# Kernel tuning notes

Measured on AMD Instinct MI355X. Metric: run time of the kernel, lower is better.

Reference implementation:

```python
import jax, jax.numpy as jnp
import numpy as np

N, E, F_IN, HID, EMB = 100000, 3200000, 128, 16, 8
NEG_SLOPE = 0.2


def _seg_softmax(logits, seg, n):
    # Numerically stable softmax over segments (per trailing channel if 2D).
    m = jax.ops.segment_max(logits, seg, num_segments=n)
    e = jnp.exp(logits - m[seg])
    s = jax.ops.segment_sum(e, seg, num_segments=n)
    return e / s[seg]


def _gatv2(x, src, dst, Wl, Wr, att, bias, t, n):
    # GATv2Conv, heads=1, add_self_loops=False, eval mode (dropout off),
    # with learnable SoftmaxAggregation replacing the sum aggregation.
    xl = x @ Wl                      # [N, C] source transform
    xr = x @ Wr                      # [N, C] target transform
    score = jnp.sum(jax.nn.leaky_relu(xl[src] + xr[dst], NEG_SLOPE) * att, axis=-1)  # [E]
    alpha = _seg_softmax(score, dst, n)          # attention softmax over incoming edges
    m = xl[src] * alpha[:, None]                 # [E, C] messages
    w = _seg_softmax(m * t, dst, n)              # SoftmaxAggregation(learn=True), per channel
    return jax.ops.segment_sum(w * m, dst, num_segments=n) + bias


def setup_inputs() -> dict:
    key = jax.random.key(0)
    ks = iter(jax.random.split(key, 32))
    r = lambda shape, s=0.1: jax.random.normal(next(ks), shape, dtype=jnp.float32) * s
    return dict(
        x=r((N, F_IN), 1.0),
        edge_index=jax.random.randint(next(ks), (2, E), 0, N, dtype=jnp.int32),
        batch=jnp.arange(N, dtype=jnp.int32),
        Wl1=r((F_IN, HID)), Wr1=r((F_IN, HID)), att1=r((HID,)), b1=r((HID,)),
        Wlin1=r((F_IN, HID)), blin1=r((HID,)),
        Wl2=r((HID, EMB)), Wr2=r((HID, EMB)), att2=r((EMB,)), b2=r((EMB,)),
        Wlin2=r((HID, EMB)), blin2=r((EMB,)),
        t=jnp.ones((1,), jnp.float32),
        W3=r((EMB, EMB)), b3=r((EMB,)),
        W4=r((EMB, 1)), b4=r((1,)),
        W5=r((1, 1)), b5=r((1,)),
        Wout=r((1, 1)), bout=r((1,)),
    )


def reference(x, edge_index, batch, Wl1, Wr1, att1, b1, Wlin1, blin1,
              Wl2, Wr2, att2, b2, Wlin2, blin2, t,
              W3, b3, W4, b4, W5, b5, Wout, bout):
    n = x.shape[0]
    src, dst = edge_index[0], edge_index[1]
    # layer 1: GATv2 + skip Linear, relu, global_add_pool
    h = _gatv2(x, src, dst, Wl1, Wr1, att1, b1, t, n) + (x @ Wlin1 + blin1)
    h = jax.nn.relu(h)
    g = jax.ops.segment_sum(h, batch, num_segments=n)  # global_add_pool (batch=arange(N))
    # layer 2: GATv2 + skip Linear on pooled tensor (as in original code), relu, pool
    h2 = _gatv2(g, src, dst, Wl2, Wr2, att2, b2, t, n) + (g @ Wlin2 + blin2)
    h2 = jax.nn.relu(h2)
    g2 = jax.ops.segment_sum(h2, batch, num_segments=n)
    # small MLP head
    z = jax.nn.relu(g2 @ W3 + b3)
    z = jax.nn.relu(z @ W4 + b4)
    z = jax.nn.relu(z @ W5 + b5)
    return jax.nn.log_sigmoid(z @ Wout + bout)
```

## Files before the change

### kernel.cpp

```cpp
#include <hip/hip_runtime.h>
#include <hip/hip_bf16.h>
#include <math.h>

#define F_IN 128
#define C1 16
#define C2 8

#define LBITS 8
#define LOCAL (1 << LBITS)
#define NB_MAX 512
#define ITEMS 16
#define EPB (256 * ITEMS)

static __device__ __forceinline__ unsigned short f2bf(float f) {
  __hip_bfloat16 h = __float2bfloat16(f);
  return *(unsigned short*)&h;
}

__global__ void bucket_hist(const int* __restrict__ dst, int* __restrict__ bcount, int E, int NB) {
  __shared__ int h[NB_MAX];
  for (int i = threadIdx.x; i < NB; i += blockDim.x) h[i] = 0;
  __syncthreads();
  int stride = gridDim.x * blockDim.x;
  int tid = blockIdx.x * blockDim.x + threadIdx.x;
  if ((E & 3) == 0) {
    const int4* d4 = (const int4*)dst;
    int n4 = E >> 2;
    for (int i = tid; i < n4; i += stride) {
      int4 d = d4[i];
      atomicAdd(&h[d.x >> LBITS], 1);
      atomicAdd(&h[d.y >> LBITS], 1);
      atomicAdd(&h[d.z >> LBITS], 1);
      atomicAdd(&h[d.w >> LBITS], 1);
    }
  } else {
    for (int e = tid; e < E; e += stride) atomicAdd(&h[dst[e] >> LBITS], 1);
  }
  __syncthreads();
  for (int i = threadIdx.x; i < NB; i += blockDim.x)
    if (h[i]) atomicAdd(&bcount[i], h[i]);
}

__global__ void bucket_scan(const int* __restrict__ bcount, int* __restrict__ bbase,
                            int* __restrict__ bcursor, int NB) {
  __shared__ int sd[NB_MAX];
  int t = threadIdx.x;
  int v = (t < NB) ? bcount[t] : 0;
  sd[t] = v;
  __syncthreads();
  int acc = v;
  for (int off = 1; off < NB_MAX; off <<= 1) {
    int u = (t >= off) ? sd[t - off] : 0;
    __syncthreads();
    acc += u;
    sd[t] = acc;
    __syncthreads();
  }
  if (t < NB) {
    int excl = acc - v;
    bbase[t] = excl;
    bcursor[t] = excl;
    if (t == NB - 1) bbase[NB] = acc;
  }
}

__global__ __launch_bounds__(256) void phaseA_lds(const int* __restrict__ src,
                                                  const int* __restrict__ dst,
                                                  int* __restrict__ bcursor,
                                                  int* __restrict__ packed, int E, int NB) {
  __shared__ int hist[NB_MAX];
  __shared__ int lbase[NB_MAX];
  __shared__ int gbase[NB_MAX];
  __shared__ int sdata[256];
  __shared__ int stage[EPB];
  __shared__ unsigned short stageb[EPB];
  int t = threadIdx.x;
  for (int i = t; i < NB; i += 256) hist[i] = 0;
  __syncthreads();
  int base = blockIdx.x * EPB;
  int vals[ITEMS];
  int bkt[ITEMS];
  bool vec = ((E & 3) == 0) && (base + EPB <= E);
  if (vec) {
    const int4* s4 = (const int4*)(src + base);
    const int4* d4 = (const int4*)(dst + base);
#pragma unroll
    for (int q = 0; q < ITEMS / 4; q++) {
      int idx = q * 256 + t;
      int4 sv = s4[idx];
      int4 dv = d4[idx];
      int ss[4] = {sv.x, sv.y, sv.z, sv.w};
      int dd[4] = {dv.x, dv.y, dv.z, dv.w};
#pragma unroll
      for (int r = 0; r < 4; r++) {
        int k = q * 4 + r;
        bkt[k] = dd[r] >> LBITS;
        vals[k] = (ss[r] << LBITS) | (dd[r] & (LOCAL - 1));
        atomicAdd(&hist[bkt[k]], 1);
      }
    }
  } else {
#pragma unroll
    for (int k = 0; k < ITEMS; k++) {
      int e = base + k * 256 + t;
      if (e < E) {
        int s = src[e];
        int d = dst[e];
        bkt[k] = d >> LBITS;
        vals[k] = (s << LBITS) | (d & (LOCAL - 1));
        atomicAdd(&hist[bkt[k]], 1);
      } else {
        bkt[k] = -1;
      }
    }
  }
  __syncthreads();
  int i0 = 2 * t, i1 = 2 * t + 1;
  int h0 = (i0 < NB) ? hist[i0] : 0;
  int h1 = (i1 < NB) ? hist[i1] : 0;
  int s2 = h0 + h1;
  sdata[t] = s2;
  __syncthreads();
  int acc = s2;
  for (int off = 1; off < 256; off <<= 1) {
    int u = (t >= off) ? sdata[t - off] : 0;
    __syncthreads();
    acc += u;
    sdata[t] = acc;
    __syncthreads();
  }
  int excl = acc - s2;
  if (i0 < NB) lbase[i0] = excl;
  if (i1 < NB) lbase[i1] = excl + h0;
  __syncthreads();
  for (int i = t; i < NB; i += 256) {
    int c = hist[i];
    gbase[i] = c ? atomicAdd(&bcursor[i], c) : 0;
    hist[i] = lbase[i];
  }
  __syncthreads();
  if (vec) {
#pragma unroll
    for (int k = 0; k < ITEMS; k++) {
      int lp = atomicAdd(&hist[bkt[k]], 1);
      stage[lp] = vals[k];
      stageb[lp] = (unsigned short)bkt[k];
    }
  } else {
#pragma unroll
    for (int k = 0; k < ITEMS; k++) {
      if (bkt[k] >= 0) {
        int lp = atomicAdd(&hist[bkt[k]], 1);
        stage[lp] = vals[k];
        stageb[lp] = (unsigned short)bkt[k];
      }
    }
  }
  __syncthreads();
  int blockE = E - base;
  if (blockE > EPB) blockE = EPB;
  for (int i = t; i < blockE; i += 256) {
    int b = stageb[i];
    packed[gbase[b] + (i - lbase[b])] = stage[i];
  }
}

__global__ void phaseB_sort(const int* __restrict__ packed, const int* __restrict__ bbase,
                            int* __restrict__ row_ptr, int* __restrict__ ssrc, int N, int E) {
  __shared__ int h[LOCAL];
  __shared__ int sd[LOCAL];
  int b = blockIdx.x;
  int t = threadIdx.x;
  int beg = bbase[b], end = bbase[b + 1];
  int node0 = b << LBITS;
  h[t] = 0;
  __syncthreads();
  for (int j = beg + t; j < end; j += blockDim.x) atomicAdd(&h[packed[j] & (LOCAL - 1)], 1);
  __syncthreads();
  int cnt = h[t];
  sd[t] = cnt;
  __syncthreads();
  int acc = cnt;
  for (int off = 1; off < LOCAL; off <<= 1) {
    int u = (t >= off) ? sd[t - off] : 0;
    __syncthreads();
    acc += u;
    sd[t] = acc;
    __syncthreads();
  }
  int myex = acc - cnt;
  int node = node0 + t;
  if (node < N) row_ptr[node] = beg + myex;
  h[t] = beg + myex;
  if (b == gridDim.x - 1 && t == 0) row_ptr[N] = E;
  __syncthreads();
  for (int j = beg + t; j < end; j += blockDim.x) {
    int v = packed[j];
    int l = v & (LOCAL - 1);
    int p = atomicAdd(&h[l], 1);
    ssrc[p] = ((v >> LBITS) << 5) | (l & 31);
  }
}

__global__ __launch_bounds__(256) void gemm3_128x16(
    const float* __restrict__ x, const float* __restrict__ Wl, const float* __restrict__ Wr,
    const float* __restrict__ Wlin, const float* __restrict__ blin,
    __hip_bfloat16* __restrict__ XLh, float* __restrict__ XR, float* __restrict__ SK, int N) {
  int bx = blockIdx.x;
  int mat = bx % 3;
  int node = (bx / 3) * 256 + threadIdx.x;
  if (node >= N) return;
  const float* __restrict__ W = (mat == 0) ? Wl : (mat == 1) ? Wr : Wlin;
  const float4* xr4 = (const float4*)(x + (size_t)node * F_IN);
  float acc[16];
#pragma unroll
  for (int c = 0; c < 16; c++) acc[c] = 0.f;
#pragma unroll 8
  for (int kk = 0; kk < F_IN / 4; kk++) {
    float4 xv = xr4[kk];
    float xs[4] = {xv.x, xv.y, xv.z, xv.w};
#pragma unroll
    for (int j = 0; j < 4; j++) {
      int k = kk * 4 + j;
#pragma unroll
      for (int c = 0; c < 16; c++) acc[c] = fmaf(xs[j], W[k * 16 + c], acc[c]);
    }
  }
  if (mat == 0) {
    unsigned int pk[8];
#pragma unroll
    for (int i = 0; i < 8; i++)
      pk[i] = (unsigned)f2bf(acc[2 * i]) | ((unsigned)f2bf(acc[2 * i + 1]) << 16);
    uint4* xlp = (uint4*)(XLh + (size_t)node * 16);
    xlp[0] = make_uint4(pk[0], pk[1], pk[2], pk[3]);
    xlp[1] = make_uint4(pk[4], pk[5], pk[6], pk[7]);
  } else if (mat == 1) {
    float4* xrp = (float4*)(XR + (size_t)node * 16);
#pragma unroll
    for (int q = 0; q < 4; q++)
      xrp[q] = make_float4(acc[4 * q], acc[4 * q + 1], acc[4 * q + 2], acc[4 * q + 3]);
  } else {
    float4* skp = (float4*)(SK + (size_t)node * 16);
#pragma unroll
    for (int q = 0; q < 4; q++)
      skp[q] = make_float4(acc[4 * q] + blin[4 * q], acc[4 * q + 1] + blin[4 * q + 1],
                           acc[4 * q + 2] + blin[4 * q + 2], acc[4 * q + 3] + blin[4 * q + 3]);
  }
}

template <int C, int POOL, bool HEAD, bool FUSEG2>
__global__ __launch_bounds__(256) void gat_layer(
    const __hip_bfloat16* __restrict__ XLh, const float* __restrict__ XR,
    const float* __restrict__ SK, const float* __restrict__ att, const float* __restrict__ bias,
    const float* __restrict__ tp, const int* __restrict__ row_ptr, const int* __restrict__ ssrc,
    float* __restrict__ H, int N,
    const float* __restrict__ P0, const float* __restrict__ P1, const float* __restrict__ P2,
    const float* __restrict__ P3, const float* __restrict__ P4, const float* __restrict__ P5,
    const float* __restrict__ P6, const float* __restrict__ P7,
    __hip_bfloat16* __restrict__ XL2h, float* __restrict__ XR2, float* __restrict__ SK2,
    float* __restrict__ out) {
  constexpr int NPB = 256 / C;
  __shared__ __align__(16) unsigned short vpool[POOL * C];
  __shared__ float ppool[POOL];
  __shared__ __align__(16) float xrl[NPB * C];
  __shared__ int nb[NPB + 1];
  __shared__ float hsh[(HEAD || FUSEG2) ? NPB * C : 1];
  __shared__ float wfuse[FUSEG2 ? 392 : 1];
  int t = threadIdx.x;
  int node0 = blockIdx.x * NPB;

  if (t <= NPB) {
    int nd = node0 + t;
    nb[t] = row_ptr[(nd < N) ? nd : N];
  }
  {
    size_t xi = (size_t)node0 * C + t;
    xrl[t] = (xi < (size_t)N * C) ? XR[xi] : 0.f;
  }
  if constexpr (FUSEG2) {
    for (int i = t; i < 392; i += 256)
      wfuse[i] = (i < 128) ? P0[i] : (i < 256) ? P1[i - 128] : (i < 384) ? P2[i - 256] : P3[i - 384];
  }
  float attr[C];
#pragma unroll
  for (int cc = 0; cc < C; cc++) attr[cc] = att[cc];
  float tval = tp[0];
  __syncthreads();

  int bbeg = nb[0];
  int nE = nb[NPB] - bbeg;
  int nCap = (nE < POOL) ? nE : POOL;
  const unsigned short* XLu = (const unsigned short*)XLh;

  for (int slot = t; slot < nCap; slot += 256) {
    int sp = ssrc[bbeg + slot];
    int s = sp >> 5;
    int g = sp & (NPB - 1);
    float v[C];
    if constexpr (C == 16) {
      const uint4* gp = (const uint4*)(XLu + (size_t)s * 16);
      uint4 a = gp[0], b = gp[1];
      *(uint4*)&vpool[slot * 16] = a;
      *(uint4*)&vpool[slot * 16 + 8] = b;
      unsigned arr[8] = {a.x, a.y, a.z, a.w, b.x, b.y, b.z, b.w};
#pragma unroll
      for (int i = 0; i < 8; i++) {
        v[2 * i] = __uint_as_float(arr[i] << 16);
        v[2 * i + 1] = __uint_as_float(arr[i] & 0xffff0000u);
      }
    } else {
      const uint4* gp = (const uint4*)(XLu + (size_t)s * 8);
      uint4 a = gp[0];
      *(uint4*)&vpool[slot * 8] = a;
      unsigned arr[4] = {a.x, a.y, a.z, a.w};
#pragma unroll
      for (int i = 0; i < 4; i++) {
        v[2 * i] = __uint_as_float(arr[i] << 16);
        v[2 * i + 1] = __uint_as_float(arr[i] & 0xffff0000u);
      }
    }
    float xr[C];
    const float4* xp = (const float4*)&xrl[g * C];
#pragma unroll
    for (int q = 0; q < C / 4; q++) {
      float4 f = xp[q];
      xr[4 * q] = f.x;
      xr[4 * q + 1] = f.y;
      xr[4 * q + 2] = f.z;
      xr[4 * q + 3] = f.w;
    }
    float p0 = 0.f, p1 = 0.f, p2 = 0.f, p3 = 0.f;
#pragma unroll
    for (int cc = 0; cc < C; cc += 4) {
      float u0 = v[cc] + xr[cc];
      float u1 = v[cc + 1] + xr[cc + 1];
      float u2 = v[cc + 2] + xr[cc + 2];
      float u3 = v[cc + 3] + xr[cc + 3];
      p0 = fmaf(fmaxf(u0, 0.2f * u0), attr[cc], p0);
      p1 = fmaf(fmaxf(u1, 0.2f * u1), attr[cc + 1], p1);
      p2 = fmaf(fmaxf(u2, 0.2f * u2), attr[cc + 2], p2);
      p3 = fmaf(fmaxf(u3, 0.2f * u3), attr[cc + 3], p3);
    }
    ppool[slot] = __expf((p0 + p1) + (p2 + p3));
  }
  __syncthreads();

  int g = t / C;
  int c = t % C;
  int base = nb[g] - bbeg;
  int deg = nb[g + 1] - nb[g];
  int capd = POOL - base;
  capd = capd < 0 ? 0 : (capd > deg ? deg : capd);

  float invS0;
  {
    float s0 = 0.f;
    for (int j = c; j < capd; j += C) s0 += ppool[base + j];
    for (int j = capd + c; j < deg; j += C) {
      int s = ssrc[bbeg + base + j] >> 5;
      float sc = 0.f;
#pragma unroll
      for (int cc = 0; cc < C; cc++) {
        float v = __bfloat162float(XLh[(size_t)s * C + cc]);
        float u = v + xrl[g * C + cc];
        sc = fmaf(fmaxf(u, 0.2f * u), attr[cc], sc);
      }
      s0 += __expf(sc);
    }
#pragma unroll
    for (int m = 1; m < C; m <<= 1) s0 += __shfl_xor(s0, m, C);
    invS0 = (deg > 0) ? 1.0f / s0 : 0.f;
    float a = invS0 * tval;
    for (int j = c; j < capd; j += C) ppool[base + j] *= a;
  }

  float S1 = 0.f, S2 = 0.f, S1b = 0.f, S2b = 0.f;
  int jj = 0;
  for (; jj + 2 <= capd; jj += 2) {
    int sl0 = base + jj;
    float v0 = __uint_as_float(((unsigned)vpool[sl0 * C + c]) << 16);
    float q0 = v0 * ppool[sl0];
    float v1 = __uint_as_float(((unsigned)vpool[(sl0 + 1) * C + c]) << 16);
    float q1 = v1 * ppool[sl0 + 1];
    float w0 = __expf(q0);
    float w1 = __expf(q1);
    S1 += w0;
    S2 = fmaf(w0, q0, S2);
    S1b += w1;
    S2b = fmaf(w1, q1, S2b);
  }
  for (; jj < capd; jj++) {
    int sl = base + jj;
    float v = __uint_as_float(((unsigned)vpool[sl * C + c]) << 16);
    float q = v * ppool[sl];
    float w = __expf(q);
    S1 += w;
    S2 = fmaf(w, q, S2);
  }
  for (; jj < deg; jj++) {
    int s = ssrc[bbeg + base + jj] >> 5;
    float sc = 0.f, vc = 0.f;
#pragma unroll
    for (int cc = 0; cc < C; cc++) {
      float v = __bfloat162float(XLh[(size_t)s * C + cc]);
      if (cc == c) vc = v;
      float u = v + xrl[g * C + cc];
      sc = fmaf(fmaxf(u, 0.2f * u), attr[cc], sc);
    }
    float p = __expf(sc);
    float q = vc * (p * invS0 * tval);
    float w = __expf(q);
    S1 += w;
    S2 = fmaf(w, q, S2);
  }
  S1 += S1b;
  S2 += S2b;

  int node = node0 + g;
  bool valid = node < N;
  float hval = 0.f;
  if (valid) {
    float td = (tval != 0.f) ? tval : 1.f;
    float gat = (deg > 0) ? (S2 / (S1 * td)) : 0.f;
    hval = fmaxf(gat + bias[c] + SK[(size_t)node * C + c], 0.f);
  }
  if constexpr (FUSEG2) {
    hsh[g * C + c] = hval;
    __syncthreads();
    if (t < NPB * 8) {
      int g2 = t >> 3, c2 = t & 7;
      int nd = node0 + g2;
      if (nd < N) {
        float a0 = 0.f, a1 = 0.f, a2 = 0.f;
#pragma unroll
        for (int k = 0; k < 16; k++) {
          float hv = hsh[g2 * 16 + k];
          a0 = fmaf(hv, wfuse[k * 8 + c2], a0);
          a1 = fmaf(hv, wfuse[128 + k * 8 + c2], a1);
          a2 = fmaf(hv, wfuse[256 + k * 8 + c2], a2);
        }
        ((unsigned short*)XL2h)[(size_t)nd * 8 + c2] = f2bf(a0);
        XR2[(size_t)nd * 8 + c2] = a1;
        SK2[(size_t)nd * 8 + c2] = a2 + wfuse[384 + c2];
      }
    }
  } else if constexpr (HEAD) {
    hsh[g * C + c] = hval;
    __syncthreads();
    if (t < NPB) {
      int nd = node0 + t;
      if (nd < N) {
        float h[8];
#pragma unroll
        for (int k = 0; k < 8; k++) h[k] = hsh[t * 8 + k];
        float s4 = 0.f;
#pragma unroll
        for (int cc = 0; cc < 8; cc++) {
          float z = P1[cc];
#pragma unroll
          for (int k = 0; k < 8; k++) z = fmaf(h[k], P0[k * 8 + cc], z);
          z = fmaxf(z, 0.f);
          s4 = fmaf(z, P2[cc], s4);
        }
        s4 = fmaxf(s4 + P3[0], 0.f);
        float s5 = fmaxf(fmaf(s4, P4[0], P5[0]), 0.f);
        float zo = fmaf(s5, P6[0], P7[0]);
        float ls;
        if (zo >= 0.f)
          ls = -log1pf(expf(-zo));
        else
          ls = zo - log1pf(expf(zo));
        out[nd] = ls;
      }
    }
  } else {
    if (valid) H[(size_t)node * C + c] = hval;
  }
}

extern "C" void kernel_launch(void* const* d_in, const int* in_sizes, int n_in,
                              void* d_out, int out_size, void* d_ws, size_t ws_size,
                              hipStream_t stream) {
  const float* x = (const float*)d_in[0];
  const int* ei = (const int*)d_in[1];
  const float* Wl1 = (const float*)d_in[3];
  const float* Wr1 = (const float*)d_in[4];
  const float* att1 = (const float*)d_in[5];
  const float* b1 = (const float*)d_in[6];
  const float* Wlin1 = (const float*)d_in[7];
  const float* blin1 = (const float*)d_in[8];
  const float* Wl2 = (const float*)d_in[9];
  const float* Wr2 = (const float*)d_in[10];
  const float* att2 = (const float*)d_in[11];
  const float* b2 = (const float*)d_in[12];
  const float* Wlin2 = (const float*)d_in[13];
  const float* blin2 = (const float*)d_in[14];
  const float* t = (const float*)d_in[15];
  const float* W3 = (const float*)d_in[16];
  const float* b3 = (const float*)d_in[17];
  const float* W4 = (const float*)d_in[18];
  const float* b4 = (const float*)d_in[19];
  const float* W5 = (const float*)d_in[20];
  const float* b5 = (const float*)d_in[21];
  const float* Wout = (const float*)d_in[22];
  const float* bout = (const float*)d_in[23];
  float* out = (float*)d_out;

  int N = in_sizes[0] / F_IN;
  int E = in_sizes[1] / 2;
  const int* src = ei;
  const int* dst = ei + E;
  int NB = (N + LOCAL - 1) >> LBITS;

  char* ws = (char*)d_ws;
  size_t off = 0;
  auto alloc = [&](size_t bytes) -> void* {
    void* p = ws + off;
    off = (off + bytes + 255) & ~(size_t)255;
    return p;
  };
  int* bcount = (int*)alloc((size_t)NB * 4);
  int* bbase = (int*)alloc((size_t)(NB + 1) * 4);
  int* bcursor = (int*)alloc((size_t)NB * 4);
  int* packed = (int*)alloc((size_t)E * 4);
  int* row_ptr = (int*)alloc((size_t)(N + 1) * 4);
  int* ssrc = (int*)alloc((size_t)E * 4);
  __hip_bfloat16* XL1 = (__hip_bfloat16*)alloc((size_t)N * C1 * 2);
  float* XR1 = (float*)alloc((size_t)N * C1 * 4);
  float* SK1 = (float*)alloc((size_t)N * C1 * 4);
  __hip_bfloat16* XL2 = (__hip_bfloat16*)alloc((size_t)N * C2 * 2);
  float* XR2 = (float*)alloc((size_t)N * C2 * 4);
  float* SK2 = (float*)alloc((size_t)N * C2 * 4);

  int nblkA = (E + EPB - 1) / EPB;
  int nodeBlk = (N + 255) / 256;

  hipMemsetAsync(bcount, 0, (size_t)NB * 4, stream);
  hipLaunchKernelGGL(bucket_hist, dim3(1024), dim3(256), 0, stream, dst, bcount, E, NB);
  hipLaunchKernelGGL(bucket_scan, dim3(1), dim3(NB_MAX), 0, stream, bcount, bbase, bcursor, NB);
  hipLaunchKernelGGL(phaseA_lds, dim3(nblkA), dim3(256), 0, stream, src, dst, bcursor, packed, E,
                     NB);
  hipLaunchKernelGGL(phaseB_sort, dim3(NB), dim3(LOCAL), 0, stream, packed, bbase, row_ptr, ssrc, N,
                     E);
  hipLaunchKernelGGL(gemm3_128x16, dim3(nodeBlk * 3), dim3(256), 0, stream, x, Wl1, Wr1,
                     Wlin1, blin1, XL1, XR1, SK1, N);
  hipLaunchKernelGGL((gat_layer<16, 640, false, true>), dim3((N + 15) / 16), dim3(256), 0, stream,
                     XL1, XR1, SK1, att1, b1, t, row_ptr, ssrc, nullptr, N, Wl2, Wr2, Wlin2, blin2,
                     nullptr, nullptr, nullptr, nullptr, XL2, XR2, SK2, nullptr);
  hipLaunchKernelGGL((gat_layer<8, 1216, true, false>), dim3((N + 31) / 32), dim3(256), 0, stream,
                     XL2, XR2, SK2, att2, b2, t, row_ptr, ssrc, nullptr, N, W3, b3, W4, b4, W5, b5,
                     Wout, bout, nullptr, nullptr, nullptr, out);
}
```

Before: 311.2 us.

## Fuse bucket histogram with layer-1 GEMM and trim GAT layer LDS usage

Merges the destination histogram kernel and the three-matrix layer-1 projection into one launch, splitting the grid by block index so both independent workloads run concurrently and one launch disappears. In the GAT layer the separate hsh shared buffer is aliased onto vpool (with an extra barrier), the per-edge rescale loop over ppool is replaced by multiplying by a scalar inside the accumulation loops, and the layer-1 pool capacity is reduced. The intent is lower LDS footprint for higher occupancy and less launch/serialization overhead, at the cost of a smaller in-LDS edge cache that may send more edges to the slow global fallback.

```diff
diff --git a/kernel.cpp b/kernel.cpp
--- a/kernel.cpp
+++ b/kernel.cpp
@@ -11,34 +11,82 @@
 #define NB_MAX 512
 #define ITEMS 16
 #define EPB (256 * ITEMS)
+#define HISTBLK 512
 
 static __device__ __forceinline__ unsigned short f2bf(float f) {
   __hip_bfloat16 h = __float2bfloat16(f);
   return *(unsigned short*)&h;
 }
 
-__global__ void bucket_hist(const int* __restrict__ dst, int* __restrict__ bcount, int E, int NB) {
-  __shared__ int h[NB_MAX];
-  for (int i = threadIdx.x; i < NB; i += blockDim.x) h[i] = 0;
-  __syncthreads();
-  int stride = gridDim.x * blockDim.x;
-  int tid = blockIdx.x * blockDim.x + threadIdx.x;
-  if ((E & 3) == 0) {
-    const int4* d4 = (const int4*)dst;
-    int n4 = E >> 2;
-    for (int i = tid; i < n4; i += stride) {
-      int4 d = d4[i];
-      atomicAdd(&h[d.x >> LBITS], 1);
-      atomicAdd(&h[d.y >> LBITS], 1);
-      atomicAdd(&h[d.z >> LBITS], 1);
-      atomicAdd(&h[d.w >> LBITS], 1);
-    }
+__global__ __launch_bounds__(256) void hist_gemm(
+    const int* __restrict__ dst, int* __restrict__ bcount, int E, int NB,
+    const float* __restrict__ x, const float* __restrict__ Wl, const float* __restrict__ Wr,
+    const float* __restrict__ Wlin, const float* __restrict__ blin,
+    __hip_bfloat16* __restrict__ XLh, float* __restrict__ XR, float* __restrict__ SK, int N) {
+  if (blockIdx.x < HISTBLK) {
+    __shared__ int h[NB_MAX];
+    for (int i = threadIdx.x; i < NB; i += blockDim.x) h[i] = 0;
+    __syncthreads();
+    int stride = HISTBLK * 256;
+    int tid = blockIdx.x * 256 + threadIdx.x;
+    if ((E & 3) == 0) {
+      const int4* d4 = (const int4*)dst;
+      int n4 = E >> 2;
+      for (int i = tid; i < n4; i += stride) {
+        int4 d = d4[i];
+        atomicAdd(&h[d.x >> LBITS], 1);
+        atomicAdd(&h[d.y >> LBITS], 1);
+        atomicAdd(&h[d.z >> LBITS], 1);
+        atomicAdd(&h[d.w >> LBITS], 1);
+      }
+    } else {
+      for (int e = tid; e < E; e += stride) atomicAdd(&h[dst[e] >> LBITS], 1);
+    }
+    __syncthreads();
+    for (int i = threadIdx.x; i < NB; i += blockDim.x)
+      if (h[i]) atomicAdd(&bcount[i], h[i]);
   } else {
-    for (int e = tid; e < E; e += stride) atomicAdd(&h[dst[e] >> LBITS], 1);
-  }
-  __syncthreads();
-  for (int i = threadIdx.x; i < NB; i += blockDim.x)
-    if (h[i]) atomicAdd(&bcount[i], h[i]);
+    int bx = blockIdx.x - HISTBLK;
+    int mat = bx % 3;
+    int node = (bx / 3) * 256 + threadIdx.x;
+    if (node >= N) return;
+    const float* __restrict__ W = (mat == 0) ? Wl : (mat == 1) ? Wr : Wlin;
+    const float4* xr4 = (const float4*)(x + (size_t)node * F_IN);
+    float acc[16];
+#pragma unroll
+    for (int c = 0; c < 16; c++) acc[c] = 0.f;
+#pragma unroll 8
+    for (int kk = 0; kk < F_IN / 4; kk++) {
+      float4 xv = xr4[kk];
+      float xs[4] = {xv.x, xv.y, xv.z, xv.w};
+#pragma unroll
+      for (int j = 0; j < 4; j++) {
+        int k = kk * 4 + j;
+#pragma unroll
+        for (int c = 0; c < 16; c++) acc[c] = fmaf(xs[j], W[k * 16 + c], acc[c]);
+      }
+    }
+    if (mat == 0) {
+      unsigned int pk[8];
+#pragma unroll
+      for (int i = 0; i < 8; i++)
+        pk[i] = (unsigned)f2bf(acc[2 * i]) | ((unsigned)f2bf(acc[2 * i + 1]) << 16);
+      uint4* xlp = (uint4*)(XLh + (size_t)node * 16);
+      xlp[0] = make_uint4(pk[0], pk[1], pk[2], pk[3]);
+      xlp[1] = make_uint4(pk[4], pk[5], pk[6], pk[7]);
+    } else if (mat == 1) {
+      float4* xrp = (float4*)(XR + (size_t)node * 16);
+#pragma unroll
+      for (int q = 0; q < 4; q++)
+        xrp[q] = make_float4(acc[4 * q], acc[4 * q + 1], acc[4 * q + 2], acc[4 * q + 3]);
+    } else {
+      float4* skp = (float4*)(SK + (size_t)node * 16);
+#pragma unroll
+      for (int q = 0; q < 4; q++)
+        skp[q] = make_float4(acc[4 * q] + blin[4 * q], acc[4 * q + 1] + blin[4 * q + 1],
+                             acc[4 * q + 2] + blin[4 * q + 2], acc[4 * q + 3] + blin[4 * q + 3]);
+    }
+  }
 }
 
 __global__ void bucket_scan(const int* __restrict__ bcount, int* __restrict__ bbase,
@@ -199,52 +247,6 @@
     int l = v & (LOCAL - 1);
     int p = atomicAdd(&h[l], 1);
     ssrc[p] = ((v >> LBITS) << 5) | (l & 31);
-  }
-}
-
-__global__ __launch_bounds__(256) void gemm3_128x16(
-    const float* __restrict__ x, const float* __restrict__ Wl, const float* __restrict__ Wr,
-    const float* __restrict__ Wlin, const float* __restrict__ blin,
-    __hip_bfloat16* __restrict__ XLh, float* __restrict__ XR, float* __restrict__ SK, int N) {
-  int bx = blockIdx.x;
-  int mat = bx % 3;
-  int node = (bx / 3) * 256 + threadIdx.x;
-  if (node >= N) return;
-  const float* __restrict__ W = (mat == 0) ? Wl : (mat == 1) ? Wr : Wlin;
-  const float4* xr4 = (const float4*)(x + (size_t)node * F_IN);
-  float acc[16];
-#pragma unroll
-  for (int c = 0; c < 16; c++) acc[c] = 0.f;
-#pragma unroll 8
-  for (int kk = 0; kk < F_IN / 4; kk++) {
-    float4 xv = xr4[kk];
-    float xs[4] = {xv.x, xv.y, xv.z, xv.w};
-#pragma unroll
-    for (int j = 0; j < 4; j++) {
-      int k = kk * 4 + j;
-#pragma unroll
-      for (int c = 0; c < 16; c++) acc[c] = fmaf(xs[j], W[k * 16 + c], acc[c]);
-    }
-  }
-  if (mat == 0) {
-    unsigned int pk[8];
-#pragma unroll
-    for (int i = 0; i < 8; i++)
-      pk[i] = (unsigned)f2bf(acc[2 * i]) | ((unsigned)f2bf(acc[2 * i + 1]) << 16);
-    uint4* xlp = (uint4*)(XLh + (size_t)node * 16);
-    xlp[0] = make_uint4(pk[0], pk[1], pk[2], pk[3]);
-    xlp[1] = make_uint4(pk[4], pk[5], pk[6], pk[7]);
-  } else if (mat == 1) {
-    float4* xrp = (float4*)(XR + (size_t)node * 16);
-#pragma unroll
-    for (int q = 0; q < 4; q++)
-      xrp[q] = make_float4(acc[4 * q], acc[4 * q + 1], acc[4 * q + 2], acc[4 * q + 3]);
-  } else {
-    float4* skp = (float4*)(SK + (size_t)node * 16);
-#pragma unroll
-    for (int q = 0; q < 4; q++)
-      skp[q] = make_float4(acc[4 * q] + blin[4 * q], acc[4 * q + 1] + blin[4 * q + 1],
-                           acc[4 * q + 2] + blin[4 * q + 2], acc[4 * q + 3] + blin[4 * q + 3]);
   }
 }
 
@@ -264,8 +266,8 @@
   __shared__ float ppool[POOL];
   __shared__ __align__(16) float xrl[NPB * C];
   __shared__ int nb[NPB + 1];
-  __shared__ float hsh[(HEAD || FUSEG2) ? NPB * C : 1];
   __shared__ float wfuse[FUSEG2 ? 392 : 1];
+  float* hsh = (float*)vpool;
   int t = threadIdx.x;
   int node0 = blockIdx.x * NPB;
 
@@ -370,18 +372,17 @@
 #pragma unroll
     for (int m = 1; m < C; m <<= 1) s0 += __shfl_xor(s0, m, C);
     invS0 = (deg > 0) ? 1.0f / s0 : 0.f;
-    float a = invS0 * tval;
-    for (int j = c; j < capd; j += C) ppool[base + j] *= a;
-  }
+  }
+  float a = invS0 * tval;
 
   float S1 = 0.f, S2 = 0.f, S1b = 0.f, S2b = 0.f;
   int jj = 0;
   for (; jj + 2 <= capd; jj += 2) {
     int sl0 = base + jj;
     float v0 = __uint_as_float(((unsigned)vpool[sl0 * C + c]) << 16);
-    float q0 = v0 * ppool[sl0];
+    float q0 = v0 * ppool[sl0] * a;
     float v1 = __uint_as_float(((unsigned)vpool[(sl0 + 1) * C + c]) << 16);
-    float q1 = v1 * ppool[sl0 + 1];
+    float q1 = v1 * ppool[sl0 + 1] * a;
     float w0 = __expf(q0);
     float w1 = __expf(q1);
     S1 += w0;
@@ -392,7 +393,7 @@
   for (; jj < capd; jj++) {
     int sl = base + jj;
     float v = __uint_as_float(((unsigned)vpool[sl * C + c]) << 16);
-    float q = v * ppool[sl];
+    float q = v * ppool[sl] * a;
     float w = __expf(q);
     S1 += w;
     S2 = fmaf(w, q, S2);
@@ -408,7 +409,7 @@
       sc = fmaf(fmaxf(u, 0.2f * u), attr[cc], sc);
     }
     float p = __expf(sc);
-    float q = vc * (p * invS0 * tval);
+    float q = vc * p * a;
     float w = __expf(q);
     S1 += w;
     S2 = fmaf(w, q, S2);
@@ -425,6 +426,7 @@
     hval = fmaxf(gat + bias[c] + SK[(size_t)node * C + c], 0.f);
   }
   if constexpr (FUSEG2) {
+    __syncthreads();
     hsh[g * C + c] = hval;
     __syncthreads();
     if (t < NPB * 8) {
@@ -445,6 +447,7 @@
       }
     }
   } else if constexpr (HEAD) {
+    __syncthreads();
     hsh[g * C + c] = hval;
     __syncthreads();
     if (t < NPB) {
@@ -536,15 +539,14 @@
   int nodeBlk = (N + 255) / 256;
 
   hipMemsetAsync(bcount, 0, (size_t)NB * 4, stream);
-  hipLaunchKernelGGL(bucket_hist, dim3(1024), dim3(256), 0, stream, dst, bcount, E, NB);
+  hipLaunchKernelGGL(hist_gemm, dim3(HISTBLK + nodeBlk * 3), dim3(256), 0, stream, dst, bcount, E,
+                     NB, x, Wl1, Wr1, Wlin1, blin1, XL1, XR1, SK1, N);
   hipLaunchKernelGGL(bucket_scan, dim3(1), dim3(NB_MAX), 0, stream, bcount, bbase, bcursor, NB);
   hipLaunchKernelGGL(phaseA_lds, dim3(nblkA), dim3(256), 0, stream, src, dst, bcursor, packed, E,
                      NB);
   hipLaunchKernelGGL(phaseB_sort, dim3(NB), dim3(LOCAL), 0, stream, packed, bbase, row_ptr, ssrc, N,
                      E);
-  hipLaunchKernelGGL(gemm3_128x16, dim3(nodeBlk * 3), dim3(256), 0, stream, x, Wl1, Wr1,
-                     Wlin1, blin1, XL1, XR1, SK1, N);
-  hipLaunchKernelGGL((gat_layer<16, 640, false, true>), dim3((N + 15) / 16), dim3(256), 0, stream,
+  hipLaunchKernelGGL((gat_layer<16, 576, false, true>), dim3((N + 15) / 16), dim3(256), 0, stream,
                      XL1, XR1, SK1, att1, b1, t, row_ptr, ssrc, nullptr, N, Wl2, Wr2, Wlin2, blin2,
                      nullptr, nullptr, nullptr, nullptr, XL2, XR2, SK2, nullptr);
   hipLaunchKernelGGL((gat_layer<8, 1216, true, false>), dim3((N + 31) / 32), dim3(256), 0, stream,
```

Result: faster. 302.7 us (-2.7%).
